# Optimization experiments

Measured on AMD Instinct MI355X. Metric: run time of the kernel, lower is better.

The kernel has to match this reference:

```python
import jax, jax.numpy as jnp
import numpy as np
from jax import lax

Q = 4          # decimation factor
N_ORDER = 8    # IIR filter order (scipy decimate default / explicit n=8)
RP = 0.05      # passband ripple in dB used by scipy.signal.decimate


def _cheby1_ba(N, rp, Wn):
    """Chebyshev type-I lowpass design, identical math to scipy.signal.cheby1."""
    eps = np.sqrt(10.0 ** (0.1 * rp) - 1.0)
    mu = np.arcsinh(1.0 / eps) / N
    k = np.arange(1, N + 1)
    theta = np.pi * (2 * k - 1) / (2 * N)
    # analog prototype poles (cheb1ap)
    p = -np.sinh(mu) * np.sin(theta) + 1j * np.cosh(mu) * np.cos(theta)
    g = np.prod(-p).real
    if N % 2 == 0:
        g /= np.sqrt(1.0 + eps ** 2)
    # frequency pre-warp (iirfilter with fs=2.0)
    fs = 2.0
    warped = 2.0 * fs * np.tan(np.pi * Wn / fs)
    # lp2lp_zpk
    p = p * warped
    g = g * warped ** N
    # bilinear_zpk
    fs2 = 2.0 * fs
    pd = (fs2 + p) / (fs2 - p)
    zd = -np.ones(N)  # N zeros at z=-1
    gd = g * np.real(1.0 / np.prod(fs2 - p))
    b = np.real(gd * np.poly(zd))
    a = np.real(np.poly(pd))
    return b, a


def _lfilter_zi(b, a):
    """Steady-state initial conditions, identical math to scipy.signal.lfilter_zi."""
    n = len(a)
    comp = np.zeros((n - 1, n - 1))
    comp[0, :] = -a[1:] / a[0]
    comp[1:, :-1] = np.eye(n - 2)
    IminusA = np.eye(n - 1) - comp.T
    B = b[1:] - a[1:] * b[0]
    return np.linalg.solve(IminusA, B)


_B_NP, _A_NP = _cheby1_ba(N_ORDER, RP, 0.8 / Q)
_ZI_NP = _lfilter_zi(_B_NP, _A_NP)


def _lfilter(b, a, x, zi):
    """IIR filter, direct-form II transposed. x: (T, M), zi: (order, M)."""
    def step(z, xt):
        yt = b[0] * xt + z[0]                       # (M,)
        z = jnp.concatenate([z[1:], jnp.zeros_like(z[:1])], axis=0) \
            + b[1:, None] * xt[None, :] - a[1:, None] * yt[None, :]
        return z, yt
    _, y = lax.scan(step, zi, x)
    return y


def _filtfilt(b, a, zi, x):
    """scipy.signal.filtfilt with padtype='odd', padlen=3*max(len(a),len(b)). x: (T, M)."""
    edge = 3 * b.shape[0]  # 27 for an order-8 filter
    left = 2.0 * x[0] - x[edge:0:-1]            # odd extension, left
    right = 2.0 * x[-1] - x[-2:-(edge + 2):-1]  # odd extension, right
    ext = jnp.concatenate([left, x, right], axis=0)
    y = _lfilter(b, a, ext, zi[:, None] * ext[0][None, :])          # forward pass
    y = _lfilter(b, a, y[::-1], zi[:, None] * y[-1][None, :])[::-1]  # backward pass
    return y[edge:-edge]


def _decimate(x):
    """scipy.signal.decimate(x, q=Q, n=8, ftype='iir', axis=-1, zero_phase=True)."""
    B_, C_, T = x.shape
    b = jnp.asarray(_B_NP, x.dtype)
    a = jnp.asarray(_A_NP, x.dtype)
    zi = jnp.asarray(_ZI_NP, x.dtype)
    xt = x.reshape(B_ * C_, T).T  # (T, M) -- time leading for lax.scan
    y = _filtfilt(b, a, zi, xt)
    y = y.T.reshape(B_, C_, T)
    return y[..., ::Q]


def setup_inputs() -> dict:
    key = jax.random.key(0)
    x = jax.random.normal(key, (32, 16, 65536), dtype=jnp.float32)
    return {"x": x}


def reference(x):
    return _decimate(x)
```

## Files before the change

kernel.cpp:

```cpp
#include <hip/hip_runtime.h>
#include <cmath>
#include <complex>

namespace {

constexpr int TLEN   = 65536;
constexpr int NCH    = 512;
constexpr int LEXT   = TLEN + 54;
constexpr int PAD    = 5;
constexpr size_t YB_ROWS = 16400;


struct Coefs {
  float b0,b1,b2,b3,b4,b5,b6,b7,b8;
  float na1,na2,na3,na4,na5,na6,na7,na8;
  float zi0,zi1,zi2,zi3,zi4,zi5,zi6,zi7;
};

#define IIR_STEP(xv, yv)                                  \
  do {                                                    \
    yv = fmaf(cf.b0, (xv), z0);                           \
    z0 = fmaf(cf.na1, yv, fmaf(cf.b1, (xv), z1));         \
    z1 = fmaf(cf.na2, yv, fmaf(cf.b2, (xv), z2));         \
    z2 = fmaf(cf.na3, yv, fmaf(cf.b3, (xv), z3));         \
    z3 = fmaf(cf.na4, yv, fmaf(cf.b4, (xv), z4));         \
    z4 = fmaf(cf.na5, yv, fmaf(cf.b5, (xv), z5));         \
    z5 = fmaf(cf.na6, yv, fmaf(cf.b6, (xv), z6));         \
    z6 = fmaf(cf.na7, yv, fmaf(cf.b7, (xv), z7));         \
    z7 = fmaf(cf.na8, yv, cf.b8 * (xv));                  \
  } while (0)

template<int QOFF, bool VEC>
__device__ __forceinline__ void run_chunk(const float* __restrict__ x,
                                          float* __restrict__ yb,
                                          const Coefs& cf,
                                          float (&lds)[3][4160],
                                          int m0, int e0, int nsub,
                                          int store_lo, int store_hi) {
  const int tid  = threadIdx.x;
  const int lane = tid & 63;
  const int vtbase = e0 - 27;
  const int mIdx = m0 + lane;
  float4* yq = reinterpret_cast<float4*>(yb);
  const int tq  = tid & 15;
  const int chb = tid >> 4;
  float4 rr0, rr1, rr2, rr3;
  float rs[16];

  auto issue = [&](int k) {
    const int vt0 = vtbase + 64 * k;
    if (VEC) {
      const float* p = x + (size_t)(m0 + chb) * TLEN + vt0 + 4 * tq;
      rr0 = *reinterpret_cast<const float4*>(p);
      rr1 = *reinterpret_cast<const float4*>(p + (size_t)16 * TLEN);
      rr2 = *reinterpret_cast<const float4*>(p + (size_t)32 * TLEN);
      rr3 = *reinterpret_cast<const float4*>(p + (size_t)48 * TLEN);
    } else {
#pragma unroll
      for (int i = 0; i < 16; ++i) {
        int idx = tid + 256 * i;
        int tl = idx & 63, ch = idx >> 6;
        int vt = vt0 + tl;
        const float* xr = x + (size_t)(m0 + ch) * TLEN;
        float v;
        if (vt < 0) v = 2.0f * xr[0] - xr[-vt];
        else if (vt >= TLEN) v = 2.0f * xr[TLEN - 1] - xr[2 * TLEN - 2 - vt];
        else v = xr[vt];
        rs[i] = v;
      }
    }
  };
  auto commit = [&](int k) {
    float* b = lds[k % 3];
    if (VEC) {
      const int base = 4 * tq * 65;
      b[base       + chb     ] = rr0.x; b[base + 65  + chb     ] = rr0.y;
      b[base + 130 + chb     ] = rr0.z; b[base + 195 + chb     ] = rr0.w;
      b[base       + chb + 16] = rr1.x; b[base + 65  + chb + 16] = rr1.y;
      b[base + 130 + chb + 16] = rr1.z; b[base + 195 + chb + 16] = rr1.w;
      b[base       + chb + 32] = rr2.x; b[base + 65  + chb + 32] = rr2.y;
      b[base + 130 + chb + 32] = rr2.z; b[base + 195 + chb + 32] = rr2.w;
      b[base       + chb + 48] = rr3.x; b[base + 65  + chb + 48] = rr3.y;
      b[base + 130 + chb + 48] = rr3.z; b[base + 195 + chb + 48] = rr3.w;
    } else {
#pragma unroll
      for (int i = 0; i < 16; ++i) {
        int idx = tid + 256 * i;
        int tl = idx & 63, ch = idx >> 6;
        b[tl * 65 + ch] = rs[i];
      }
    }
  };

  issue(0); commit(0);
  issue(1); commit(1);

  float z0 = 0, z1 = 0, z2 = 0, z3 = 0, z4 = 0, z5 = 0, z6 = 0, z7 = 0;
  float4 oq = make_float4(0.f, 0.f, 0.f, 0.f);

  for (int k = 0; k < nsub; ++k) {
    __syncthreads();
    if (k == 0 && tid < 64) {
      float x0 = lds[0][lane];
      z0 = cf.zi0 * x0; z1 = cf.zi1 * x0; z2 = cf.zi2 * x0; z3 = cf.zi3 * x0;
      z4 = cf.zi4 * x0; z5 = cf.zi5 * x0; z6 = cf.zi6 * x0; z7 = cf.zi7 * x0;
    }
    if (k + 2 < nsub) issue(k + 2);
    if (tid < 64) {
      const float* tile = lds[k % 3];
#pragma unroll
      for (int tl = 0; tl < 64; ++tl) {
        float xin = tile[tl * 65 + lane];
        float yv; IIR_STEP(xin, yv);
        if (QOFF == 1) {
          if (k == 0 && tl < 3) yb[2048 + mIdx * 4 + tl + 1] = yv;
        }
        const int q = (tl + QOFF) & 3;
        if (q == 0) oq.x = yv;
        else if (q == 1) oq.y = yv;
        else if (q == 2) oq.z = yv;
        else {
          oq.w = yv;
          const int step = 64 * k + tl;
          if (step >= store_lo && step <= store_hi)
            yq[(size_t)((e0 + step + 5) >> 2) * 512 + mIdx] = oq;
        }
      }
    }
    if (k + 2 < nsub) commit(k + 2);
  }
}

__global__ __launch_bounds__(256) void k_fwd2(const float* __restrict__ x,
                                              float* __restrict__ yb, Coefs cf) {
  __shared__ float lds[3][4160];
  const int c  = blockIdx.x;
  const int m0 = blockIdx.y * 64;
  if (c == 0)
    run_chunk<1, false>(x, yb, cf, lds, m0, 0, 8, 6, 510);
  else if (c == 128)
    run_chunk<0, false>(x, yb, cf, lds, m0, 65283, 5, 255, 307);
  else
    run_chunk<0, true>(x, yb, cf, lds, m0, 512 * c - 253, 12, 255, 763);
}

__global__ __launch_bounds__(256) void k_bwd(const float* __restrict__ yb,
                                             float* __restrict__ ot2, Coefs cf) {
  const int m = blockIdx.y * 256 + threadIdx.x;
  const int c = blockIdx.x;
  const int own_lo = 256 * c;
  float z0, z1, z2, z3, z4, z5, z6, z7;
  int g_begin;
  if (c <= 1) {
    float y0 = yb[(size_t)16398 * 2048 + (size_t)m * 4 + 2];
    z0 = cf.zi0 * y0; z1 = cf.zi1 * y0; z2 = cf.zi2 * y0; z3 = cf.zi3 * y0;
    z4 = cf.zi4 * y0; z5 = cf.zi5 * y0; z6 = cf.zi6 * y0; z7 = cf.zi7 * y0;
#pragma unroll
    for (int s = 65594; s >= 65584; --s) {
      float yin = yb[(size_t)(s >> 2) * 2048 + (size_t)m * 4 + (s & 3)];
      float wv; IIR_STEP(yin, wv);
      (void)wv;
    }
    g_begin = 16395;
  } else {
    g_begin = 16463 - 64 * c;
    float y0 = yb[(size_t)g_begin * 2048 + (size_t)m * 4 + 3];
    z0 = cf.zi0 * y0; z1 = cf.zi1 * y0; z2 = cf.zi2 * y0; z3 = cf.zi3 * y0;
    z4 = cf.zi4 * y0; z5 = cf.zi5 * y0; z6 = cf.zi6 * y0; z7 = cf.zi7 * y0;
  }
  const int g_stop = max(1, 16334 - 64 * c);
  const float4* yv = reinterpret_cast<const float4*>(yb);
  auto ld = [&](int r) {
    int rr = r < 0 ? 0 : r;
    return yv[(size_t)rr * 512 + m];
  };
  float4 b0 = ld(g_begin), b1 = ld(g_begin - 1), b2 = ld(g_begin - 2), b3 = ld(g_begin - 3);
  float4 b4 = ld(g_begin - 4), b5 = ld(g_begin - 5), b6 = ld(g_begin - 6), b7 = ld(g_begin - 7);
  for (int g = g_begin; g >= g_stop; g -= 4) {
    float4 c0 = b0, c1 = b1, c2 = b2, c3 = b3;
    b0 = b4; b1 = b5; b2 = b6; b3 = b7;
    b4 = ld(g - 8); b5 = ld(g - 9); b6 = ld(g - 10); b7 = ld(g - 11);
    float4 pack;
#pragma unroll
    for (int j = 0; j < 4; ++j) {
      float4 q = (j == 0) ? c0 : (j == 1) ? c1 : (j == 2) ? c2 : c3;
      float w3, w2, w1, w0;
      IIR_STEP(q.w, w3);
      IIR_STEP(q.z, w2);
      IIR_STEP(q.y, w1);
      IIR_STEP(q.x, w0);
      (void)w3; (void)w2; (void)w1;
      if (j == 0) pack.w = w0;
      else if (j == 1) pack.z = w0;
      else if (j == 2) pack.y = w0;
      else pack.x = w0;
    }
    if (65594 - 4 * g >= own_lo && g >= 11 && g <= 16391)
      *reinterpret_cast<float4*>(ot2 + (size_t)((g - 11) >> 2) * 2048 + (size_t)m * 4) = pack;
  }
}

__global__ __launch_bounds__(256) void k_outT(const float* __restrict__ ot2,
                                              float* __restrict__ out) {
  __shared__ float4 lds4[64 * 65];
  const int q0 = blockIdx.x * 64;
  const int m0 = blockIdx.y * 64;
  const int tid = threadIdx.x;
#pragma unroll
  for (int i = 0; i < 16; ++i) {
    int idx = tid + i * 256;
    int ql = idx >> 6;
    int ml = idx & 63;
    lds4[ql * 65 + ml] = *reinterpret_cast<const float4*>(
        ot2 + (size_t)(q0 + ql) * 2048 + (size_t)(m0 + ml) * 4);
  }
  __syncthreads();
#pragma unroll
  for (int i = 0; i < 16; ++i) {
    int idx = tid + i * 256;
    int ml = idx >> 6;
    int ql = idx & 63;
    float4 v = lds4[ql * 65 + ml];
    *reinterpret_cast<float4*>(
        out + (size_t)(m0 + ml) * 16384 + (size_t)(q0 + ql) * 4) = v;
  }
}

static void solve8(double Mm[8][9], double* zi) {
  for (int col = 0; col < 8; ++col) {
    int piv = col;
    for (int r = col + 1; r < 8; ++r)
      if (std::fabs(Mm[r][col]) > std::fabs(Mm[piv][col])) piv = r;
    if (piv != col)
      for (int j = 0; j < 9; ++j) { double t = Mm[col][j]; Mm[col][j] = Mm[piv][j]; Mm[piv][j] = t; }
    double d = Mm[col][col];
    for (int j = col; j < 9; ++j) Mm[col][j] /= d;
    for (int r = 0; r < 8; ++r)
      if (r != col) {
        double f = Mm[r][col];
        if (f != 0.0)
          for (int j = col; j < 9; ++j) Mm[r][j] -= f * Mm[col][j];
      }
  }
  for (int i = 0; i < 8; ++i) zi[i] = Mm[i][8];
}

static Coefs make_coefs() {
  using cd = std::complex<double>;
  const int N = 8;
  const double rp = 0.05, Wn = 0.8 / 4.0;
  double eps = std::sqrt(std::pow(10.0, 0.1 * rp) - 1.0);
  double mu = std::asinh(1.0 / eps) / N;
  cd p[8];
  for (int i = 0; i < N; ++i) {
    double th = M_PI * (2.0 * (i + 1) - 1.0) / (2.0 * N);
    p[i] = cd(-std::sinh(mu) * std::sin(th), std::cosh(mu) * std::cos(th));
  }
  cd pr(1.0, 0.0);
  for (int i = 0; i < N; ++i) pr *= -p[i];
  double g = pr.real();
  g /= std::sqrt(1.0 + eps * eps);
  const double fs = 2.0;
  double warped = 2.0 * fs * std::tan(M_PI * Wn / fs);
  for (int i = 0; i < N; ++i) p[i] *= warped;
  g *= std::pow(warped, (double)N);
  const double fs2 = 2.0 * fs;
  cd pd[8], dpr(1.0, 0.0);
  for (int i = 0; i < N; ++i) {
    pd[i] = (cd(fs2, 0.0) + p[i]) / (cd(fs2, 0.0) - p[i]);
    dpr *= (cd(fs2, 0.0) - p[i]);
  }
  double gd = g * (cd(1.0, 0.0) / dpr).real();
  static const double binom[9] = {1, 8, 28, 56, 70, 56, 28, 8, 1};
  double b[9], a[9];
  for (int i = 0; i < 9; ++i) b[i] = gd * binom[i];
  cd cp[9]; cp[0] = cd(1, 0);
  for (int i = 1; i < 9; ++i) cp[i] = cd(0, 0);
  for (int i = 0; i < N; ++i)
    for (int j = i + 1; j >= 1; --j) cp[j] -= pd[i] * cp[j - 1];
  for (int i = 0; i < 9; ++i) a[i] = cp[i].real();
  double Mm[8][9];
  for (int i = 0; i < 8; ++i) {
    for (int j = 0; j < 9; ++j) Mm[i][j] = 0.0;
    Mm[i][0] += a[i + 1];
    Mm[i][i] += 1.0;
    if (i < 7) Mm[i][i + 1] = -1.0;
    Mm[i][8] = b[i + 1] - a[i + 1] * b[0];
  }
  double zi[8];
  solve8(Mm, zi);
  Coefs cf;
  cf.b0 = (float)b[0]; cf.b1 = (float)b[1]; cf.b2 = (float)b[2]; cf.b3 = (float)b[3];
  cf.b4 = (float)b[4]; cf.b5 = (float)b[5]; cf.b6 = (float)b[6]; cf.b7 = (float)b[7];
  cf.b8 = (float)b[8];
  cf.na1 = (float)(-a[1]); cf.na2 = (float)(-a[2]); cf.na3 = (float)(-a[3]);
  cf.na4 = (float)(-a[4]); cf.na5 = (float)(-a[5]); cf.na6 = (float)(-a[6]);
  cf.na7 = (float)(-a[7]); cf.na8 = (float)(-a[8]);
  cf.zi0 = (float)zi[0]; cf.zi1 = (float)zi[1]; cf.zi2 = (float)zi[2]; cf.zi3 = (float)zi[3];
  cf.zi4 = (float)zi[4]; cf.zi5 = (float)zi[5]; cf.zi6 = (float)zi[6]; cf.zi7 = (float)zi[7];
  return cf;
}

}

extern "C" void kernel_launch(void* const* d_in, const int* in_sizes, int n_in,
                              void* d_out, int out_size, void* d_ws, size_t ws_size,
                              hipStream_t stream) {
  (void)in_sizes; (void)n_in; (void)out_size; (void)ws_size;
  const float* x = (const float*)d_in[0];
  float* out = (float*)d_out;
  float* yb  = (float*)d_ws;
  float* ot2 = yb + YB_ROWS * 2048;
  Coefs cf = make_coefs();
  hipLaunchKernelGGL(k_fwd2, dim3(129, NCH / 64), dim3(256), 0, stream, x, yb, cf);
  hipLaunchKernelGGL(k_bwd, dim3(257, 2), dim3(256), 0, stream, yb, ot2, cf);
  hipLaunchKernelGGL(k_outT, dim3(4096 / 64, NCH / 64), dim3(256), 0, stream, ot2, out);
}
```

Baseline: 311.5 us.

## Use single-wave forward blocks with double-buffered LDS and no barriers

New measurement: 353.9 us. 1.14x slower.

```diff
diff --git a/kernel.cpp b/kernel.cpp
--- a/kernel.cpp
+++ b/kernel.cpp
@@ -6,9 +6,8 @@
 
 constexpr int TLEN   = 65536;
 constexpr int NCH    = 512;
-constexpr int LEXT   = TLEN + 54;
-constexpr int PAD    = 5;
 constexpr size_t YB_ROWS = 16400;
+constexpr int PITCH  = 68;
 
 
 struct Coefs {
@@ -30,118 +29,104 @@
     z7 = fmaf(cf.na8, yv, cf.b8 * (xv));                  \
   } while (0)
 
-template<int QOFF, bool VEC>
-__device__ __forceinline__ void run_chunk(const float* __restrict__ x,
-                                          float* __restrict__ yb,
-                                          const Coefs& cf,
-                                          float (&lds)[3][4160],
-                                          int m0, int e0, int nsub,
-                                          int store_lo, int store_hi) {
-  const int tid  = threadIdx.x;
-  const int lane = tid & 63;
+template<int QOFF>
+__device__ __forceinline__ void run_chunk1(const float* __restrict__ x,
+                                           float* __restrict__ yb,
+                                           const Coefs& cf,
+                                           float (&lds)[2][64 * PITCH],
+                                           int m0, int e0, int nsub,
+                                           int store_lo, int store_hi) {
+  const int lane   = threadIdx.x;
   const int vtbase = e0 - 27;
-  const int mIdx = m0 + lane;
+  const int mIdx   = m0 + lane;
   float4* yq = reinterpret_cast<float4*>(yb);
-  const int tq  = tid & 15;
-  const int chb = tid >> 4;
-  float4 rr0, rr1, rr2, rr3;
-  float rs[16];
-
+  const int tq  = lane & 15;
+  const int chb = lane >> 4;
+  float4 rr[16];
+
+  auto interior = [&](int k) {
+    const int vt0 = vtbase + 64 * k;
+    return vt0 >= 0 && vt0 + 63 < TLEN;
+  };
   auto issue = [&](int k) {
+    if (!interior(k)) return;
     const int vt0 = vtbase + 64 * k;
-    if (VEC) {
-      const float* p = x + (size_t)(m0 + chb) * TLEN + vt0 + 4 * tq;
-      rr0 = *reinterpret_cast<const float4*>(p);
-      rr1 = *reinterpret_cast<const float4*>(p + (size_t)16 * TLEN);
-      rr2 = *reinterpret_cast<const float4*>(p + (size_t)32 * TLEN);
-      rr3 = *reinterpret_cast<const float4*>(p + (size_t)48 * TLEN);
-    } else {
-#pragma unroll
-      for (int i = 0; i < 16; ++i) {
-        int idx = tid + 256 * i;
-        int tl = idx & 63, ch = idx >> 6;
-        int vt = vt0 + tl;
-        const float* xr = x + (size_t)(m0 + ch) * TLEN;
-        float v;
-        if (vt < 0) v = 2.0f * xr[0] - xr[-vt];
-        else if (vt >= TLEN) v = 2.0f * xr[TLEN - 1] - xr[2 * TLEN - 2 - vt];
-        else v = xr[vt];
-        rs[i] = v;
-      }
-    }
+    const float* p = x + (size_t)(m0 + chb) * TLEN + vt0 + 4 * tq;
+#pragma unroll
+    for (int pp = 0; pp < 16; ++pp)
+      rr[pp] = *reinterpret_cast<const float4*>(p + (size_t)(4 * pp) * TLEN);
   };
   auto commit = [&](int k) {
-    float* b = lds[k % 3];
-    if (VEC) {
-      const int base = 4 * tq * 65;
-      b[base       + chb     ] = rr0.x; b[base + 65  + chb     ] = rr0.y;
-      b[base + 130 + chb     ] = rr0.z; b[base + 195 + chb     ] = rr0.w;
-      b[base       + chb + 16] = rr1.x; b[base + 65  + chb + 16] = rr1.y;
-      b[base + 130 + chb + 16] = rr1.z; b[base + 195 + chb + 16] = rr1.w;
-      b[base       + chb + 32] = rr2.x; b[base + 65  + chb + 32] = rr2.y;
-      b[base + 130 + chb + 32] = rr2.z; b[base + 195 + chb + 32] = rr2.w;
-      b[base       + chb + 48] = rr3.x; b[base + 65  + chb + 48] = rr3.y;
-      b[base + 130 + chb + 48] = rr3.z; b[base + 195 + chb + 48] = rr3.w;
+    float* b = lds[k & 1];
+    if (interior(k)) {
+#pragma unroll
+      for (int pp = 0; pp < 16; ++pp)
+        *reinterpret_cast<float4*>(&b[(chb + 4 * pp) * PITCH + 4 * tq]) = rr[pp];
     } else {
-#pragma unroll
-      for (int i = 0; i < 16; ++i) {
-        int idx = tid + 256 * i;
-        int tl = idx & 63, ch = idx >> 6;
-        b[tl * 65 + ch] = rs[i];
-      }
+      const int vt = vtbase + 64 * k + lane;
+      const bool lo = vt < 0, hi = vt >= TLEN;
+      const int idx  = lo ? -vt : (hi ? 2 * TLEN - 2 - vt : vt);
+      const int eidx = hi ? TLEN - 1 : 0;
+      const float esc = (lo || hi) ? 2.0f : 0.0f;
+      const float msc = (lo || hi) ? -1.0f : 1.0f;
+      const float* xr = x + (size_t)m0 * TLEN;
+#pragma unroll 8
+      for (int ch = 0; ch < 64; ++ch, xr += TLEN)
+        b[ch * PITCH + lane] = fmaf(msc, xr[idx], esc * xr[eidx]);
     }
   };
 
   issue(0); commit(0);
-  issue(1); commit(1);
 
   float z0 = 0, z1 = 0, z2 = 0, z3 = 0, z4 = 0, z5 = 0, z6 = 0, z7 = 0;
   float4 oq = make_float4(0.f, 0.f, 0.f, 0.f);
 
   for (int k = 0; k < nsub; ++k) {
-    __syncthreads();
-    if (k == 0 && tid < 64) {
-      float x0 = lds[0][lane];
+    if (k + 1 < nsub) issue(k + 1);
+    const float* tile = lds[k & 1] + lane * PITCH;
+    if (k == 0) {
+      float x0 = tile[0];
       z0 = cf.zi0 * x0; z1 = cf.zi1 * x0; z2 = cf.zi2 * x0; z3 = cf.zi3 * x0;
       z4 = cf.zi4 * x0; z5 = cf.zi5 * x0; z6 = cf.zi6 * x0; z7 = cf.zi7 * x0;
     }
-    if (k + 2 < nsub) issue(k + 2);
-    if (tid < 64) {
-      const float* tile = lds[k % 3];
-#pragma unroll
-      for (int tl = 0; tl < 64; ++tl) {
-        float xin = tile[tl * 65 + lane];
-        float yv; IIR_STEP(xin, yv);
+#pragma unroll
+    for (int j = 0; j < 16; ++j) {
+      const float4 xv = *reinterpret_cast<const float4*>(tile + 4 * j);
+      const float xs[4] = {xv.x, xv.y, xv.z, xv.w};
+#pragma unroll
+      for (int d = 0; d < 4; ++d) {
+        float yv; IIR_STEP(xs[d], yv);
         if (QOFF == 1) {
-          if (k == 0 && tl < 3) yb[2048 + mIdx * 4 + tl + 1] = yv;
+          if (k == 0 && j == 0 && d < 3)
+            yb[2048 + (size_t)mIdx * 4 + d + 1] = yv;
         }
-        const int q = (tl + QOFF) & 3;
-        if (q == 0) oq.x = yv;
-        else if (q == 1) oq.y = yv;
-        else if (q == 2) oq.z = yv;
+        const int qq = (4 * j + d + QOFF) & 3;
+        if (qq == 0) oq.x = yv;
+        else if (qq == 1) oq.y = yv;
+        else if (qq == 2) oq.z = yv;
         else {
           oq.w = yv;
-          const int step = 64 * k + tl;
+          const int step = 64 * k + 4 * j + d;
           if (step >= store_lo && step <= store_hi)
             yq[(size_t)((e0 + step + 5) >> 2) * 512 + mIdx] = oq;
         }
       }
     }
-    if (k + 2 < nsub) commit(k + 2);
-  }
-}
-
-__global__ __launch_bounds__(256) void k_fwd2(const float* __restrict__ x,
-                                              float* __restrict__ yb, Coefs cf) {
-  __shared__ float lds[3][4160];
+    if (k + 1 < nsub) commit(k + 1);
+  }
+}
+
+__global__ __launch_bounds__(64) void k_fwd3(const float* __restrict__ x,
+                                             float* __restrict__ yb, Coefs cf) {
+  __shared__ float lds[2][64 * PITCH];
   const int c  = blockIdx.x;
   const int m0 = blockIdx.y * 64;
   if (c == 0)
-    run_chunk<1, false>(x, yb, cf, lds, m0, 0, 8, 6, 510);
-  else if (c == 128)
-    run_chunk<0, false>(x, yb, cf, lds, m0, 65283, 5, 255, 307);
+    run_chunk1<1>(x, yb, cf, lds, m0, 0, 8, 6, 510);
+  else if (c == 127)
+    run_chunk1<0>(x, yb, cf, lds, m0, 512 * 127 - 253, 13, 255, 819);
   else
-    run_chunk<0, true>(x, yb, cf, lds, m0, 512 * c - 253, 12, 255, 763);
+    run_chunk1<0>(x, yb, cf, lds, m0, 512 * c - 253, 12, 255, 763);
 }
 
 __global__ __launch_bounds__(256) void k_bwd(const float* __restrict__ yb,
@@ -312,7 +297,7 @@
   float* yb  = (float*)d_ws;
   float* ot2 = yb + YB_ROWS * 2048;
   Coefs cf = make_coefs();
-  hipLaunchKernelGGL(k_fwd2, dim3(129, NCH / 64), dim3(256), 0, stream, x, yb, cf);
+  hipLaunchKernelGGL(k_fwd3, dim3(128, NCH / 64), dim3(64), 0, stream, x, yb, cf);
   hipLaunchKernelGGL(k_bwd, dim3(257, 2), dim3(256), 0, stream, yb, ot2, cf);
   hipLaunchKernelGGL(k_outT, dim3(4096 / 64, NCH / 64), dim3(256), 0, stream, ot2, out);
 }
```

## Fuse backward IIR pass with output transpose and double-buffer forward tiles

Applied to the files above, without the earlier changes.

After: 292.2 us. -6.2%, faster.

```diff
diff --git a/kernel.cpp b/kernel.cpp
--- a/kernel.cpp
+++ b/kernel.cpp
@@ -6,8 +6,6 @@
 
 constexpr int TLEN   = 65536;
 constexpr int NCH    = 512;
-constexpr int LEXT   = TLEN + 54;
-constexpr int PAD    = 5;
 constexpr size_t YB_ROWS = 16400;
 
 
@@ -34,7 +32,7 @@
 __device__ __forceinline__ void run_chunk(const float* __restrict__ x,
                                           float* __restrict__ yb,
                                           const Coefs& cf,
-                                          float (&lds)[3][4160],
+                                          float (&lds)[2][4160],
                                           int m0, int e0, int nsub,
                                           int store_lo, int store_hi) {
   const int tid  = threadIdx.x;
@@ -71,7 +69,7 @@
     }
   };
   auto commit = [&](int k) {
-    float* b = lds[k % 3];
+    float* b = lds[k & 1];
     if (VEC) {
       const int base = 4 * tq * 65;
       b[base       + chb     ] = rr0.x; b[base + 65  + chb     ] = rr0.y;
@@ -93,21 +91,20 @@
   };
 
   issue(0); commit(0);
-  issue(1); commit(1);
 
   float z0 = 0, z1 = 0, z2 = 0, z3 = 0, z4 = 0, z5 = 0, z6 = 0, z7 = 0;
   float4 oq = make_float4(0.f, 0.f, 0.f, 0.f);
 
   for (int k = 0; k < nsub; ++k) {
+    if (k + 1 < nsub) issue(k + 1);
     __syncthreads();
     if (k == 0 && tid < 64) {
       float x0 = lds[0][lane];
       z0 = cf.zi0 * x0; z1 = cf.zi1 * x0; z2 = cf.zi2 * x0; z3 = cf.zi3 * x0;
       z4 = cf.zi4 * x0; z5 = cf.zi5 * x0; z6 = cf.zi6 * x0; z7 = cf.zi7 * x0;
     }
-    if (k + 2 < nsub) issue(k + 2);
     if (tid < 64) {
-      const float* tile = lds[k % 3];
+      const float* tile = lds[k & 1];
 #pragma unroll
       for (int tl = 0; tl < 64; ++tl) {
         float xin = tile[tl * 65 + lane];
@@ -127,13 +124,13 @@
         }
       }
     }
-    if (k + 2 < nsub) commit(k + 2);
+    if (k + 1 < nsub) commit(k + 1);
   }
 }
 
 __global__ __launch_bounds__(256) void k_fwd2(const float* __restrict__ x,
                                               float* __restrict__ yb, Coefs cf) {
-  __shared__ float lds[3][4160];
+  __shared__ float lds[2][4160];
   const int c  = blockIdx.x;
   const int m0 = blockIdx.y * 64;
   if (c == 0)
@@ -144,14 +141,15 @@
     run_chunk<0, true>(x, yb, cf, lds, m0, 512 * c - 253, 12, 255, 763);
 }
 
-__global__ __launch_bounds__(256) void k_bwd(const float* __restrict__ yb,
-                                             float* __restrict__ ot2, Coefs cf) {
-  const int m = blockIdx.y * 256 + threadIdx.x;
-  const int c = blockIdx.x;
-  const int own_lo = 256 * c;
+__global__ __launch_bounds__(256) void k_bwd2(const float* __restrict__ yb,
+                                              float* __restrict__ out, Coefs cf) {
+  __shared__ float wl[256 * 65];
+  const int c   = blockIdx.x;
+  const int tid = threadIdx.x;
+  const int m   = blockIdx.y * 256 + tid;
   float z0, z1, z2, z3, z4, z5, z6, z7;
   int g_begin;
-  if (c <= 1) {
+  if (c == 255) {
     float y0 = yb[(size_t)16398 * 2048 + (size_t)m * 4 + 2];
     z0 = cf.zi0 * y0; z1 = cf.zi1 * y0; z2 = cf.zi2 * y0; z3 = cf.zi3 * y0;
     z4 = cf.zi4 * y0; z5 = cf.zi5 * y0; z6 = cf.zi6 * y0; z7 = cf.zi7 * y0;
@@ -163,12 +161,13 @@
     }
     g_begin = 16395;
   } else {
-    g_begin = 16463 - 64 * c;
+    g_begin = 64 * c + 139;
     float y0 = yb[(size_t)g_begin * 2048 + (size_t)m * 4 + 3];
     z0 = cf.zi0 * y0; z1 = cf.zi1 * y0; z2 = cf.zi2 * y0; z3 = cf.zi3 * y0;
     z4 = cf.zi4 * y0; z5 = cf.zi5 * y0; z6 = cf.zi6 * y0; z7 = cf.zi7 * y0;
   }
-  const int g_stop = max(1, 16334 - 64 * c);
+  const int g_stop = 64 * c + 11;
+  const int g_hi   = 64 * c + 71;
   const float4* yv = reinterpret_cast<const float4*>(yb);
   auto ld = [&](int r) {
     int rr = r < 0 ? 0 : r;
@@ -195,34 +194,25 @@
       else if (j == 2) pack.y = w0;
       else pack.x = w0;
     }
-    if (65594 - 4 * g >= own_lo && g >= 11 && g <= 16391)
-      *reinterpret_cast<float4*>(ot2 + (size_t)((g - 11) >> 2) * 2048 + (size_t)m * 4) = pack;
-  }
-}
-
-__global__ __launch_bounds__(256) void k_outT(const float* __restrict__ ot2,
-                                              float* __restrict__ out) {
-  __shared__ float4 lds4[64 * 65];
-  const int q0 = blockIdx.x * 64;
-  const int m0 = blockIdx.y * 64;
-  const int tid = threadIdx.x;
+    if (g <= g_hi) {
+      const int cb = g - 11 - 64 * c;
+      wl[tid * 65 + cb    ] = pack.x;
+      wl[tid * 65 + cb + 1] = pack.y;
+      wl[tid * 65 + cb + 2] = pack.z;
+      wl[tid * 65 + cb + 3] = pack.w;
+    }
+  }
+  __syncthreads();
+  const int colb = 64 * c;
 #pragma unroll
   for (int i = 0; i < 16; ++i) {
     int idx = tid + i * 256;
-    int ql = idx >> 6;
-    int ml = idx & 63;
-    lds4[ql * 65 + ml] = *reinterpret_cast<const float4*>(
-        ot2 + (size_t)(q0 + ql) * 2048 + (size_t)(m0 + ml) * 4);
-  }
-  __syncthreads();
-#pragma unroll
-  for (int i = 0; i < 16; ++i) {
-    int idx = tid + i * 256;
-    int ml = idx >> 6;
-    int ql = idx & 63;
-    float4 v = lds4[ql * 65 + ml];
+    int ch  = idx >> 4;
+    int f4  = idx & 15;
+    float4 v = make_float4(wl[ch * 65 + 4 * f4],     wl[ch * 65 + 4 * f4 + 1],
+                           wl[ch * 65 + 4 * f4 + 2], wl[ch * 65 + 4 * f4 + 3]);
     *reinterpret_cast<float4*>(
-        out + (size_t)(m0 + ml) * 16384 + (size_t)(q0 + ql) * 4) = v;
+        out + (size_t)(blockIdx.y * 256 + ch) * 16384 + colb + 4 * f4) = v;
   }
 }
 
@@ -310,9 +300,7 @@
   const float* x = (const float*)d_in[0];
   float* out = (float*)d_out;
   float* yb  = (float*)d_ws;
-  float* ot2 = yb + YB_ROWS * 2048;
   Coefs cf = make_coefs();
   hipLaunchKernelGGL(k_fwd2, dim3(129, NCH / 64), dim3(256), 0, stream, x, yb, cf);
-  hipLaunchKernelGGL(k_bwd, dim3(257, 2), dim3(256), 0, stream, yb, ot2, cf);
-  hipLaunchKernelGGL(k_outT, dim3(4096 / 64, NCH / 64), dim3(256), 0, stream, ot2, out);
-}
+  hipLaunchKernelGGL(k_bwd2, dim3(256, 2), dim3(256), 0, stream, yb, out, cf);
+}
```
